# Kernel optimization log

Measured on AMD Instinct MI355X. Metric: run time of the kernel, lower is better.

Reference implementation:

```python
import jax, jax.numpy as jnp
import numpy as np

TEMPERATURE = 0.07
NORMALIZE = True
NEG_INF = -1e30


def setup_inputs() -> dict:
    key = jax.random.key(0)
    features = jax.random.normal(key, (8192, 512), dtype=jnp.float32)
    return {"features": features}


def reference(features):
    # features: [B, D]
    B = features.shape[0]
    if NORMALIZE:
        norm = jnp.linalg.norm(features, axis=1, keepdims=True)
        features = features / jnp.maximum(norm, 1e-12)
    # [B, B] similarity matrix
    sim = jnp.matmul(features, features.T) / TEMPERATURE

    # default SimCLR labels: arange(B//2) repeated twice -> pair (i, i + B//2)
    half = jnp.arange(B // 2, dtype=jnp.int32)
    labels = jnp.concatenate([half, half])
    eq = labels[None, :] == labels[:, None]          # [B, B]
    diag = jnp.eye(B, dtype=bool)
    mask_pos = eq & ~diag                            # positives per row

    # Original per-row CE: logits = cat(pos_sims, neg_sims) (= all j != i),
    # target index 0 = FIRST positive (lowest column index). Loss_i =
    # logsumexp_{j != i}(sim[i, j]) - sim[i, first_pos_i].
    sim_masked = jnp.where(diag, NEG_INF, sim)
    lse = jax.scipy.special.logsumexp(sim_masked, axis=1)   # [B]

    first_pos = jnp.argmax(mask_pos, axis=1)                 # first True per row
    pos_sim = jnp.take_along_axis(sim, first_pos[:, None], axis=1)[:, 0]

    has_pos = jnp.any(mask_pos, axis=1)
    losses = jnp.where(has_pos, lse - pos_sim, 0.0)
    count = jnp.maximum(jnp.sum(has_pos.astype(jnp.float32)), 1.0)
    return jnp.sum(losses) / count
```

## Files before the change

### kernel.cpp

```cpp
#include <hip/hip_runtime.h>
#include <hip/hip_bf16.h>
#include <stdint.h>

#define BATCH 8192
#define DIM   512
#define BM    256
#define NT    (BATCH / BM)
#define NPAIR (NT * (NT + 1) / 2)

#define FEAT_SCALE 4.5398164f
#define LN2        0.69314718055994531f

typedef __attribute__((ext_vector_type(8))) short short8;
typedef __attribute__((ext_vector_type(4))) float f32x4;

__device__ __forceinline__ void gld_lds16(const void* g, void* l) {
  __builtin_amdgcn_global_load_lds(
      (__attribute__((address_space(1))) void*)(uintptr_t)g,
      (__attribute__((address_space(3))) void*)(uintptr_t)l,
      16, 0, 0);
}

__global__ __launch_bounds__(256) void normalize_bf16(
    const float* __restrict__ x, __hip_bfloat16* __restrict__ o,
    float* __restrict__ rowsum) {
  const int wv = threadIdx.x >> 6, lane = threadIdx.x & 63;
  const int row = blockIdx.x * 4 + wv;
  if (lane == 0) rowsum[row] = 0.0f;
  const float4* xr = (const float4*)(x + (size_t)row * DIM);
  const float4 v0 = xr[lane];
  const float4 v1 = xr[lane + 64];
  float ss = v0.x * v0.x + v0.y * v0.y + v0.z * v0.z + v0.w * v0.w +
             v1.x * v1.x + v1.y * v1.y + v1.z * v1.z + v1.w * v1.w;
#pragma unroll
  for (int m = 32; m > 0; m >>= 1) ss += __shfl_xor(ss, m, 64);
  const float inv = FEAT_SCALE / fmaxf(sqrtf(ss), 1e-12f);
  ushort4 p0, p1;
  p0.x = __bfloat16_as_ushort(__float2bfloat16(v0.x * inv));
  p0.y = __bfloat16_as_ushort(__float2bfloat16(v0.y * inv));
  p0.z = __bfloat16_as_ushort(__float2bfloat16(v0.z * inv));
  p0.w = __bfloat16_as_ushort(__float2bfloat16(v0.w * inv));
  p1.x = __bfloat16_as_ushort(__float2bfloat16(v1.x * inv));
  p1.y = __bfloat16_as_ushort(__float2bfloat16(v1.y * inv));
  p1.z = __bfloat16_as_ushort(__float2bfloat16(v1.z * inv));
  p1.w = __bfloat16_as_ushort(__float2bfloat16(v1.w * inv));
  ushort4* orow = (ushort4*)(o + (size_t)row * DIM);
  orow[lane]      = p0;
  orow[lane + 64] = p1;
}

__global__ __launch_bounds__(512, 2) void sim_lse_kernel(
    const __hip_bfloat16* __restrict__ F, float* __restrict__ rowsum,
    float* __restrict__ possim) {
  extern __shared__ char smem[];
  float* colAcc = (float*)(smem + 131072);

  const int pr = blockIdx.x;
  int by = (int)((65.0f - sqrtf(65.0f * 65.0f - 8.0f * (float)pr)) * 0.5f);
  if (by > NT - 1) by = NT - 1;
  if (by < 0) by = 0;
  while ((by + 1) * (65 - (by + 1)) / 2 <= pr) ++by;
  while (by * (65 - by) / 2 > pr) --by;
  const int bx = by + (pr - by * (65 - by) / 2);
  const bool diagTile = (bx == by);
  const bool hasPos = (bx == by + NT / 2);

  const int rowB = by * BM;
  const int colB = bx * BM;

  const int tid  = threadIdx.x;
  const int lane = tid & 63;
  const int wv   = tid >> 6;
  const int q    = lane >> 4;
  const int l15  = lane & 15;
  const int waveM = wv >> 2;
  const int waveN = wv & 3;

  const int r0 = tid >> 3, c0 = tid & 7;
  const int csrc = c0 ^ (r0 & 7);
  const __hip_bfloat16* gAp = F + (size_t)(rowB + r0) * DIM + csrc * 8;
  const __hip_bfloat16* gBp = F + (size_t)(colB + r0) * DIM + csrc * 8;

#define STAGE_A(Tn) do {                                                      \
    const int kk_ = ((Tn) & 7) * 64;                                          \
    char* d_ = smem + ((Tn) & 1) * 65536 + wv * 1024;                         \
    gld_lds16(gAp + kk_,                 d_);                                 \
    gld_lds16(gAp + kk_ + 32768,         d_ + 8192);                          \
    gld_lds16(gAp + kk_ + 65536,         d_ + 16384);                         \
    gld_lds16(gAp + kk_ + 98304,         d_ + 24576);                         \
  } while (0)
#define STAGE_B(Tn) do {                                                      \
    const int kk_ = ((Tn) & 7) * 64;                                          \
    char* d_ = smem + ((Tn) & 1) * 65536 + 32768 + wv * 1024;                 \
    gld_lds16(gBp + kk_,                 d_);                                 \
    gld_lds16(gBp + kk_ + 32768,         d_ + 8192);                          \
    gld_lds16(gBp + kk_ + 65536,         d_ + 16384);                         \
    gld_lds16(gBp + kk_ + 98304,         d_ + 24576);                         \
  } while (0)

  const int cs0 = ((q)     ^ (l15 & 7)) * 16;
  const int cs1 = ((4 + q) ^ (l15 & 7)) * 16;
  const int abase = waveM * 16384 + l15 * 128;
  const int bbase = 32768 + (waveN >> 1) * 16384 + ((waveN & 1) * 64 + l15) * 128;

  short8 a[4], b[4];
  f32x4 acc[8][4] = {};

#define RD_B(BF_, CS_) do {                                                   \
    const char* p_ = smem + (BF_) * 65536 + bbase + (CS_);                    \
    b[0] = *(const short8*)(p_);                                              \
    b[1] = *(const short8*)(p_ + 2048);                                       \
    b[2] = *(const short8*)(p_ + 4096);                                       \
    b[3] = *(const short8*)(p_ + 6144);                                       \
  } while (0)
#define RD_A(BF_, LH_, CS_) do {                                              \
    const char* p_ = smem + (BF_) * 65536 + abase + (LH_) * 8192 + (CS_);     \
    a[0] = *(const short8*)(p_);                                              \
    a[1] = *(const short8*)(p_ + 2048);                                       \
    a[2] = *(const short8*)(p_ + 4096);                                       \
    a[3] = *(const short8*)(p_ + 6144);                                       \
  } while (0)
#define MFMA16(LH_) do {                                                      \
    __builtin_amdgcn_s_setprio(1);                                            \
    _Pragma("unroll")                                                         \
    for (int m_ = 0; m_ < 4; ++m_)                                            \
      _Pragma("unroll")                                                       \
      for (int n_ = 0; n_ < 4; ++n_)                                          \
        acc[(LH_) * 4 + m_][n_] = __builtin_amdgcn_mfma_f32_16x16x32_bf16(    \
            a[m_], b[n_], acc[(LH_) * 4 + m_][n_], 0, 0, 0);                  \
    __builtin_amdgcn_s_setprio(0);                                            \
    __builtin_amdgcn_sched_barrier(0);                                        \
  } while (0)

  if (tid < 256) colAcc[tid] = 0.0f;

  STAGE_A(0); STAGE_B(0);
  asm volatile("s_waitcnt vmcnt(0)" ::: "memory");
  __builtin_amdgcn_s_barrier();

#pragma unroll
  for (int T = 0; T < 8; ++T) {
    const int bf = T & 1;
    RD_B(bf, cs0); RD_A(bf, 0, cs0);
    if (T < 7) STAGE_A(T + 1);
    MFMA16(0);
    RD_A(bf, 1, cs0);
    if (T < 7) STAGE_B(T + 1);
    MFMA16(1);
    RD_B(bf, cs1); RD_A(bf, 0, cs1);
    MFMA16(0);
    RD_A(bf, 1, cs1);
    MFMA16(1);
    asm volatile("s_waitcnt vmcnt(0)" ::: "memory");
    __builtin_amdgcn_s_barrier();
  }

  float* redBuf = (float*)smem;
  float cp[4] = {0.f, 0.f, 0.f, 0.f};
  f32x4 rp[8];

#pragma unroll
  for (int mi = 0; mi < 8; ++mi) {
    f32x4 r = {0.f, 0.f, 0.f, 0.f};
#pragma unroll
    for (int ni = 0; ni < 4; ++ni) {
      const int lc = waveN * 64 + ni * 16 + l15;
#pragma unroll
      for (int rr = 0; rr < 4; ++rr) {
        const int lr = waveM * 128 + mi * 16 + q * 4 + rr;
        const float s = acc[mi][ni][rr];
        float e = exp2f(s);
        if (diagTile && lc == lr) e = 0.0f;
        r[rr] += e;
        cp[ni] += e;
        if (hasPos && lc == lr) {
          possim[rowB + lr] = s;
          possim[rowB + lr + BATCH / 2] = s;
        }
      }
    }
    rp[mi] = r;
  }

  {
    float* wb = redBuf + (waveN * 16 + l15) * 260 + waveM * 128 + q * 4;
#pragma unroll
    for (int mi = 0; mi < 8; ++mi) *(f32x4*)(wb + mi * 16) = rp[mi];
  }

  if (!diagTile) {
#pragma unroll
    for (int ni = 0; ni < 4; ++ni) {
      float c = cp[ni];
      c += __shfl_xor(c, 16, 64);
      c += __shfl_xor(c, 32, 64);
      if (q == 0) atomicAdd(&colAcc[waveN * 64 + ni * 16 + l15], c);
    }
  }
  asm volatile("s_waitcnt lgkmcnt(0)" ::: "memory");
  __builtin_amdgcn_s_barrier();

  {
    const int row = tid >> 1, half = tid & 1;
    const float* bp = redBuf + half * 32 * 260 + row;
    float ssum = 0.f;
#pragma unroll
    for (int j = 0; j < 32; ++j) ssum += bp[j * 260];
    ssum += __shfl_xor(ssum, 1, 64);
    if (half == 0) atomicAdd(&rowsum[rowB + row], ssum);
  }
  if (!diagTile && tid < 256)
    atomicAdd(&rowsum[colB + tid], colAcc[tid]);
}

__global__ __launch_bounds__(1024) void finalize_kernel(
    const float* __restrict__ rowsum, const float* __restrict__ possim,
    float* __restrict__ out) {
  float acc = 0.0f;
  for (int i = threadIdx.x; i < BATCH; i += 1024)
    acc += __logf(rowsum[i]) - possim[i] * LN2;
#pragma unroll
  for (int m = 32; m > 0; m >>= 1) acc += __shfl_xor(acc, m, 64);
  __shared__ float ws[16];
  const int lane = threadIdx.x & 63, wv = threadIdx.x >> 6;
  if (lane == 0) ws[wv] = acc;
  __syncthreads();
  if (threadIdx.x == 0) {
    float tot = 0.0f;
#pragma unroll
    for (int k = 0; k < 16; ++k) tot += ws[k];
    out[0] = tot * (1.0f / (float)BATCH);
  }
}

extern "C" void kernel_launch(void* const* d_in, const int* in_sizes, int n_in,
                              void* d_out, int out_size, void* d_ws, size_t ws_size,
                              hipStream_t stream) {
  const float* x = (const float*)d_in[0];
  float* out = (float*)d_out;

  __hip_bfloat16* Fb = (__hip_bfloat16*)d_ws;
  float* rowsum = (float*)((char*)d_ws + (size_t)BATCH * DIM * sizeof(__hip_bfloat16));
  float* possim = rowsum + BATCH;

  static bool attr_done = false;
  if (!attr_done) {
    (void)hipFuncSetAttribute(reinterpret_cast<const void*>(sim_lse_kernel),
                              hipFuncAttributeMaxDynamicSharedMemorySize, 132096);
    attr_done = true;
  }

  normalize_bf16<<<BATCH / 4, 256, 0, stream>>>(x, Fb, rowsum);
  sim_lse_kernel<<<NPAIR, 512, 132096, stream>>>(Fb, rowsum, possim);
  finalize_kernel<<<1, 1024, 0, stream>>>(rowsum, possim, out);
}
```

Before: 120.5 us.

## Split each triangle tile into two 128-row blocks with single-buffered staging

Each 256x256 upper-triangle tile is now split into two 128x256 blocks of 256 threads. Staging drops to a single 48KB static LDS buffer with a sync before and after each K step, and column partial sums go straight to global atomics instead of an LDS accumulator. The aim is more resident blocks and better balance across the grid. In exchange it loses double-buffered load/compute overlap, loads every B tile twice, and issues more global atomics on rowsum.

```diff
diff --git a/kernel.cpp b/kernel.cpp
--- a/kernel.cpp
+++ b/kernel.cpp
@@ -7,6 +7,7 @@
 #define BM    256
 #define NT    (BATCH / BM)
 #define NPAIR (NT * (NT + 1) / 2)
+#define NBLK  (NPAIR * 2)
 
 #define FEAT_SCALE 4.5398164f
 #define LN2        0.69314718055994531f
@@ -49,13 +50,14 @@
   orow[lane + 64] = p1;
 }
 
-__global__ __launch_bounds__(512, 2) void sim_lse_kernel(
+__global__ __launch_bounds__(256, 2) void sim_lse_kernel(
     const __hip_bfloat16* __restrict__ F, float* __restrict__ rowsum,
     float* __restrict__ possim) {
-  extern __shared__ char smem[];
-  float* colAcc = (float*)(smem + 131072);
-
-  const int pr = blockIdx.x;
+  __shared__ char smem[49152];
+
+  const int t  = blockIdx.x;
+  const int pr = t >> 1;
+  const int hb = t & 1;
   int by = (int)((65.0f - sqrtf(65.0f * 65.0f - 8.0f * (float)pr)) * 0.5f);
   if (by > NT - 1) by = NT - 1;
   if (by < 0) by = 0;
@@ -65,7 +67,7 @@
   const bool diagTile = (bx == by);
   const bool hasPos = (bx == by + NT / 2);
 
-  const int rowB = by * BM;
+  const int rowB = by * BM + hb * 128;
   const int colB = bx * BM;
 
   const int tid  = threadIdx.x;
@@ -73,86 +75,59 @@
   const int wv   = tid >> 6;
   const int q    = lane >> 4;
   const int l15  = lane & 15;
-  const int waveM = wv >> 2;
-  const int waveN = wv & 3;
 
   const int r0 = tid >> 3, c0 = tid & 7;
   const int csrc = c0 ^ (r0 & 7);
-  const __hip_bfloat16* gAp = F + (size_t)(rowB + r0) * DIM + csrc * 8;
-  const __hip_bfloat16* gBp = F + (size_t)(colB + r0) * DIM + csrc * 8;
-
-#define STAGE_A(Tn) do {                                                      \
-    const int kk_ = ((Tn) & 7) * 64;                                          \
-    char* d_ = smem + ((Tn) & 1) * 65536 + wv * 1024;                         \
-    gld_lds16(gAp + kk_,                 d_);                                 \
-    gld_lds16(gAp + kk_ + 32768,         d_ + 8192);                          \
-    gld_lds16(gAp + kk_ + 65536,         d_ + 16384);                         \
-    gld_lds16(gAp + kk_ + 98304,         d_ + 24576);                         \
-  } while (0)
-#define STAGE_B(Tn) do {                                                      \
-    const int kk_ = ((Tn) & 7) * 64;                                          \
-    char* d_ = smem + ((Tn) & 1) * 65536 + 32768 + wv * 1024;                 \
-    gld_lds16(gBp + kk_,                 d_);                                 \
-    gld_lds16(gBp + kk_ + 32768,         d_ + 8192);                          \
-    gld_lds16(gBp + kk_ + 65536,         d_ + 16384);                         \
-    gld_lds16(gBp + kk_ + 98304,         d_ + 24576);                         \
+  const __hip_bfloat16* gA = F + (size_t)(rowB + r0) * DIM + csrc * 8;
+  const __hip_bfloat16* gB = F + (size_t)(colB + r0) * DIM + csrc * 8;
+
+#define STAGE(T_) do {                                                        \
+    const int ko_ = (T_) * 64;                                                \
+    gld_lds16(gA + ko_,                smem + wv * 1024);                     \
+    gld_lds16(gA + ko_ + 32 * DIM,     smem + 4096 + wv * 1024);              \
+    gld_lds16(gA + ko_ + 64 * DIM,     smem + 8192 + wv * 1024);              \
+    gld_lds16(gA + ko_ + 96 * DIM,     smem + 12288 + wv * 1024);             \
+    gld_lds16(gB + ko_,                smem + 16384 + wv * 1024);             \
+    gld_lds16(gB + ko_ + 32 * DIM,     smem + 20480 + wv * 1024);             \
+    gld_lds16(gB + ko_ + 64 * DIM,     smem + 24576 + wv * 1024);             \
+    gld_lds16(gB + ko_ + 96 * DIM,     smem + 28672 + wv * 1024);             \
+    gld_lds16(gB + ko_ + 128 * DIM,    smem + 32768 + wv * 1024);             \
+    gld_lds16(gB + ko_ + 160 * DIM,    smem + 36864 + wv * 1024);             \
+    gld_lds16(gB + ko_ + 192 * DIM,    smem + 40960 + wv * 1024);             \
+    gld_lds16(gB + ko_ + 224 * DIM,    smem + 45056 + wv * 1024);             \
   } while (0)
 
   const int cs0 = ((q)     ^ (l15 & 7)) * 16;
   const int cs1 = ((4 + q) ^ (l15 & 7)) * 16;
-  const int abase = waveM * 16384 + l15 * 128;
-  const int bbase = 32768 + (waveN >> 1) * 16384 + ((waveN & 1) * 64 + l15) * 128;
+  const int arow = l15 * 128;
+  const int brow = 16384 + (wv * 64 + l15) * 128;
 
   short8 a[4], b[4];
   f32x4 acc[8][4] = {};
 
-#define RD_B(BF_, CS_) do {                                                   \
-    const char* p_ = smem + (BF_) * 65536 + bbase + (CS_);                    \
-    b[0] = *(const short8*)(p_);                                              \
-    b[1] = *(const short8*)(p_ + 2048);                                       \
-    b[2] = *(const short8*)(p_ + 4096);                                       \
-    b[3] = *(const short8*)(p_ + 6144);                                       \
-  } while (0)
-#define RD_A(BF_, LH_, CS_) do {                                              \
-    const char* p_ = smem + (BF_) * 65536 + abase + (LH_) * 8192 + (CS_);     \
-    a[0] = *(const short8*)(p_);                                              \
-    a[1] = *(const short8*)(p_ + 2048);                                       \
-    a[2] = *(const short8*)(p_ + 4096);                                       \
-    a[3] = *(const short8*)(p_ + 6144);                                       \
-  } while (0)
-#define MFMA16(LH_) do {                                                      \
-    __builtin_amdgcn_s_setprio(1);                                            \
-    _Pragma("unroll")                                                         \
-    for (int m_ = 0; m_ < 4; ++m_)                                            \
-      _Pragma("unroll")                                                       \
-      for (int n_ = 0; n_ < 4; ++n_)                                          \
-        acc[(LH_) * 4 + m_][n_] = __builtin_amdgcn_mfma_f32_16x16x32_bf16(    \
-            a[m_], b[n_], acc[(LH_) * 4 + m_][n_], 0, 0, 0);                  \
-    __builtin_amdgcn_s_setprio(0);                                            \
-    __builtin_amdgcn_sched_barrier(0);                                        \
-  } while (0)
-
-  if (tid < 256) colAcc[tid] = 0.0f;
-
-  STAGE_A(0); STAGE_B(0);
-  asm volatile("s_waitcnt vmcnt(0)" ::: "memory");
-  __builtin_amdgcn_s_barrier();
-
-#pragma unroll
   for (int T = 0; T < 8; ++T) {
-    const int bf = T & 1;
-    RD_B(bf, cs0); RD_A(bf, 0, cs0);
-    if (T < 7) STAGE_A(T + 1);
-    MFMA16(0);
-    RD_A(bf, 1, cs0);
-    if (T < 7) STAGE_B(T + 1);
-    MFMA16(1);
-    RD_B(bf, cs1); RD_A(bf, 0, cs1);
-    MFMA16(0);
-    RD_A(bf, 1, cs1);
-    MFMA16(1);
-    asm volatile("s_waitcnt vmcnt(0)" ::: "memory");
-    __builtin_amdgcn_s_barrier();
+    STAGE(T);
+    __syncthreads();
+#pragma unroll
+    for (int ks = 0; ks < 2; ++ks) {
+      const int cs = ks ? cs1 : cs0;
+#pragma unroll
+      for (int ni = 0; ni < 4; ++ni)
+        b[ni] = *(const short8*)(smem + brow + ni * 2048 + cs);
+#pragma unroll
+      for (int H = 0; H < 2; ++H) {
+#pragma unroll
+        for (int mi = 0; mi < 4; ++mi)
+          a[mi] = *(const short8*)(smem + arow + H * 8192 + mi * 2048 + cs);
+#pragma unroll
+        for (int mi = 0; mi < 4; ++mi)
+#pragma unroll
+          for (int ni = 0; ni < 4; ++ni)
+            acc[H * 4 + mi][ni] = __builtin_amdgcn_mfma_f32_16x16x32_bf16(
+                a[mi], b[ni], acc[H * 4 + mi][ni], 0, 0, 0);
+      }
+    }
+    __syncthreads();
   }
 
   float* redBuf = (float*)smem;
@@ -164,16 +139,16 @@
     f32x4 r = {0.f, 0.f, 0.f, 0.f};
 #pragma unroll
     for (int ni = 0; ni < 4; ++ni) {
-      const int lc = waveN * 64 + ni * 16 + l15;
+      const int lc = wv * 64 + ni * 16 + l15;
 #pragma unroll
       for (int rr = 0; rr < 4; ++rr) {
-        const int lr = waveM * 128 + mi * 16 + q * 4 + rr;
+        const int lr = mi * 16 + q * 4 + rr;
         const float s = acc[mi][ni][rr];
         float e = exp2f(s);
-        if (diagTile && lc == lr) e = 0.0f;
+        if (diagTile && lc == hb * 128 + lr) e = 0.0f;
         r[rr] += e;
         cp[ni] += e;
-        if (hasPos && lc == lr) {
+        if (hasPos && lc == hb * 128 + lr) {
           possim[rowB + lr] = s;
           possim[rowB + lr + BATCH / 2] = s;
         }
@@ -183,7 +158,7 @@
   }
 
   {
-    float* wb = redBuf + (waveN * 16 + l15) * 260 + waveM * 128 + q * 4;
+    float* wb = redBuf + (wv * 16 + l15) * 132 + q * 4;
 #pragma unroll
     for (int mi = 0; mi < 8; ++mi) *(f32x4*)(wb + mi * 16) = rp[mi];
   }
@@ -194,23 +169,20 @@
       float c = cp[ni];
       c += __shfl_xor(c, 16, 64);
       c += __shfl_xor(c, 32, 64);
-      if (q == 0) atomicAdd(&colAcc[waveN * 64 + ni * 16 + l15], c);
+      if (q == 0) atomicAdd(&rowsum[colB + wv * 64 + ni * 16 + l15], c);
     }
   }
-  asm volatile("s_waitcnt lgkmcnt(0)" ::: "memory");
-  __builtin_amdgcn_s_barrier();
+  __syncthreads();
 
   {
     const int row = tid >> 1, half = tid & 1;
-    const float* bp = redBuf + half * 32 * 260 + row;
+    const float* bp = redBuf + half * 32 * 132 + row;
     float ssum = 0.f;
 #pragma unroll
-    for (int j = 0; j < 32; ++j) ssum += bp[j * 260];
+    for (int j = 0; j < 32; ++j) ssum += bp[j * 132];
     ssum += __shfl_xor(ssum, 1, 64);
     if (half == 0) atomicAdd(&rowsum[rowB + row], ssum);
   }
-  if (!diagTile && tid < 256)
-    atomicAdd(&rowsum[colB + tid], colAcc[tid]);
 }
 
 __global__ __launch_bounds__(1024) void finalize_kernel(
@@ -243,14 +215,7 @@
   float* rowsum = (float*)((char*)d_ws + (size_t)BATCH * DIM * sizeof(__hip_bfloat16));
   float* possim = rowsum + BATCH;
 
-  static bool attr_done = false;
-  if (!attr_done) {
-    (void)hipFuncSetAttribute(reinterpret_cast<const void*>(sim_lse_kernel),
-                              hipFuncAttributeMaxDynamicSharedMemorySize, 132096);
-    attr_done = true;
-  }
-
   normalize_bf16<<<BATCH / 4, 256, 0, stream>>>(x, Fb, rowsum);
-  sim_lse_kernel<<<NPAIR, 512, 132096, stream>>>(Fb, rowsum, possim);
+  sim_lse_kernel<<<NBLK, 256, 0, stream>>>(Fb, rowsum, possim);
   finalize_kernel<<<1, 1024, 0, stream>>>(rowsum, possim, out);
 }
```

New measurement: 117.6 us. 1.03x faster.
